# Kernel optimization log

Hardware: AMD Instinct MI355X
Metric: run time of the kernel (lower is better)

The kernel has to match this reference:

```python
import math
import jax, jax.numpy as jnp
import numpy as np

B, S, D = 2, 2048, 1024
N_HEADS, D_KV = 16, 64
INNER = N_HEADS * D_KV
NUM_BUCKETS = 32
MAX_DISTANCE = 128


def _relative_position_bucket(relative_position, num_buckets=NUM_BUCKETS, max_distance=MAX_DISTANCE):
    # bidirectional (encoder) variant
    nb = num_buckets // 2
    rel_buckets = (relative_position > 0).astype(jnp.int32) * nb
    rp = jnp.abs(relative_position)
    max_exact = nb // 2
    is_small = rp < max_exact
    rp_safe = jnp.maximum(rp, 1)  # avoid log(0); selected away by where
    rp_if_large = max_exact + (
        jnp.log(rp_safe.astype(jnp.float32) / max_exact)
        / math.log(max_distance / max_exact)
        * (nb - max_exact)
    ).astype(jnp.int32)
    rp_if_large = jnp.minimum(rp_if_large, nb - 1)
    return rel_buckets + jnp.where(is_small, rp, rp_if_large)


def compute_bias(rel_bias, q_len, k_len):
    ctx = jnp.arange(q_len)[:, None]
    mem = jnp.arange(k_len)[None, :]
    buckets = _relative_position_bucket(mem - ctx)  # [q_len, k_len]
    values = rel_bias[buckets]                      # [q_len, k_len, H]
    return jnp.transpose(values, (2, 0, 1))[None]   # [1, H, q_len, k_len]


def setup_inputs() -> dict:
    key = jax.random.key(0)
    ks = jax.random.split(key, 6)
    s = 1.0 / math.sqrt(D)
    return {
        "hidden_states": jax.random.normal(ks[0], (B, S, D), jnp.float32),
        "wq": jax.random.normal(ks[1], (D, INNER), jnp.float32) * s,
        "wk": jax.random.normal(ks[2], (D, INNER), jnp.float32) * s,
        "wv": jax.random.normal(ks[3], (D, INNER), jnp.float32) * s,
        "wo": jax.random.normal(ks[4], (INNER, D), jnp.float32) * s,
        "rel_bias": jax.random.normal(ks[5], (NUM_BUCKETS, N_HEADS), jnp.float32) * 0.1,
    }


def reference(hidden_states, wq, wk, wv, wo, rel_bias):
    b, s, _ = hidden_states.shape

    def shape(x):  # [b, s, inner] -> [b, h, s, d_kv]
        return x.reshape(b, s, N_HEADS, D_KV).transpose(0, 2, 1, 3)

    q = shape(hidden_states @ wq)  # note: T5 has NO 1/sqrt(d) scaling
    k = shape(hidden_states @ wk)
    v = shape(hidden_states @ wv)

    scores = jnp.einsum("bhqd,bhkd->bhqk", q, k)
    position_bias = compute_bias(rel_bias, s, s)
    scores = scores + position_bias
    attn = jax.nn.softmax(scores.astype(jnp.float32), axis=-1).astype(scores.dtype)

    out = jnp.einsum("bhqk,bhkd->bhqd", attn, v)
    out = out.transpose(0, 2, 1, 3).reshape(b, s, INNER)
    return out @ wo
```

## Files before the change

kernel.cpp:

```cpp
#include <hip/hip_runtime.h>
#include <hip/hip_bf16.h>

#define B_ 2
#define S_ 2048
#define D_ 1024
#define H_ 16
#define DKV_ 64
#define INNER_ 1024
#define M_ (B_*S_)

typedef unsigned short ushort_t;
typedef unsigned int u32;
typedef __bf16 bf16x8 __attribute__((ext_vector_type(8)));
typedef __bf16 bf16x4 __attribute__((ext_vector_type(4)));
typedef float f32x4 __attribute__((ext_vector_type(4)));

#define VMCNT0 asm volatile("s_waitcnt vmcnt(0)" ::: "memory")
#define LOG2E 1.4426950408889634f

__device__ __forceinline__ unsigned short f2bf(float f) {
    unsigned int u = __builtin_bit_cast(unsigned int, f);
    unsigned int r = (u + 0x7fffu + ((u >> 16) & 1u)) >> 16;
    return (unsigned short)r;
}

__device__ __forceinline__ void gload16(const ushort_t* g, ushort_t* l) {
    __builtin_amdgcn_global_load_lds(
        (const __attribute__((address_space(1))) u32*)g,
        (__attribute__((address_space(3))) u32*)l, 16, 0, 0);
}

__global__ __launch_bounds__(256) void cvt_bf16(const float* __restrict__ in,
                                                unsigned short* __restrict__ out, int n) {
    int i = (blockIdx.x * 256 + threadIdx.x) * 4;
    if (i < n) {
        float4 v = *(const float4*)&in[i];
        ushort4 o;
        o.x = f2bf(v.x); o.y = f2bf(v.y); o.z = f2bf(v.z); o.w = f2bf(v.w);
        *(ushort4*)&out[i] = o;
    }
}

__global__ __launch_bounds__(256) void transp_bf16(
        const float* __restrict__ s0, const float* __restrict__ s1,
        const float* __restrict__ s2, const float* __restrict__ s3,
        unsigned short* __restrict__ d0, unsigned short* __restrict__ d1,
        unsigned short* __restrict__ d2, unsigned short* __restrict__ d3) {
    const float* srcs[4] = {s0, s1, s2, s3};
    unsigned short* dsts[4] = {d0, d1, d2, d3};
    const float* src = srcs[blockIdx.z];
    unsigned short* dst = dsts[blockIdx.z];
    __shared__ float t[64][65];
    int k0 = blockIdx.y * 64, n0 = blockIdx.x * 64;
    for (int i = threadIdx.x; i < 4096; i += 256) {
        int r = i >> 6, c = i & 63;
        t[r][c] = src[(k0 + r) * 1024 + n0 + c];
    }
    __syncthreads();
    for (int i = threadIdx.x; i < 4096; i += 256) {
        int r = i >> 6, c = i & 63;
        dst[(n0 + r) * 1024 + k0 + c] = f2bf(t[c][r]);
    }
}

__global__ __launch_bounds__(256) void bias_kernel(const float* __restrict__ rb,
                                                   float* __restrict__ btab) {
    int idx = blockIdx.x * 256 + threadIdx.x;
    int h = idx >> 12, pos = idx & 4095;
    int rel = pos - 2048;
    int bb = rel > 0 ? 16 : 0;
    int rp = rel < 0 ? -rel : rel;
    int bucket;
    if (rp < 8) bucket = bb + rp;
    else {
        int v = 8 + (int)(logf((float)rp * 0.125f) / 2.7725887f * 8.0f);
        bucket = bb + (v < 15 ? v : 15);
    }
    btab[idx] = rb[bucket * 16 + h] * LOG2E;
}

__global__ __launch_bounds__(256) void gemm_qkv(const ushort_t* __restrict__ A,
        const ushort_t* __restrict__ WQ, const ushort_t* __restrict__ WK, const ushort_t* __restrict__ WV,
        ushort_t* __restrict__ Qb, ushort_t* __restrict__ Kb, ushort_t* __restrict__ Vtb) {
    __shared__ alignas(16) ushort_t As[128][64];
    __shared__ alignas(16) ushort_t Bs[128][64];
    int tid = threadIdx.x, wid = tid >> 6, lane = tid & 63;
    int linear = blockIdx.x;
    int swz = (linear & 7) * 96 + (linear >> 3);
    int m0 = (swz / 24) * 128;
    int nblk = swz % 24;
    int sel = nblk >> 3;
    const ushort_t* Bt = sel == 0 ? WQ : (sel == 1 ? WK : WV);
    int n0 = (nblk & 7) * 128;
    int lr = lane & 15, lg = lane >> 4;
    int wm = (wid >> 1) * 64, wn = (wid & 1) * 64;
    int srow = tid >> 3, sp = tid & 7;
    int scol = (sp ^ (srow & 7)) * 8;
    int cR0 = (lg ^ (lr & 7)) * 8;
    int cR1 = ((4 + lg) ^ (lr & 7)) * 8;
    const ushort_t* Abase = A + (size_t)m0 * 1024 + scol;
    const ushort_t* Bbase = Bt + (size_t)n0 * 1024 + scol;
    f32x4 acc[4][4] = {};
    for (int kt = 0; kt < 1024; kt += 64) {
        #pragma unroll
        for (int j = 0; j < 4; ++j) {
            int row = j * 32 + srow;
            gload16(Abase + row * 1024 + kt, &As[0][0] + (j * 256 + tid) * 8);
            gload16(Bbase + row * 1024 + kt, &Bs[0][0] + (j * 256 + tid) * 8);
        }
        VMCNT0;
        __syncthreads();
        bf16x8 af[4][2], bfr[4][2];
        #pragma unroll
        for (int t = 0; t < 4; ++t) {
            af[t][0]  = *(const bf16x8*)&As[wm + t * 16 + lr][cR0];
            af[t][1]  = *(const bf16x8*)&As[wm + t * 16 + lr][cR1];
            bfr[t][0] = *(const bf16x8*)&Bs[wn + t * 16 + lr][cR0];
            bfr[t][1] = *(const bf16x8*)&Bs[wn + t * 16 + lr][cR1];
        }
        #pragma unroll
        for (int hh = 0; hh < 2; ++hh)
            #pragma unroll
            for (int i2 = 0; i2 < 4; ++i2)
                #pragma unroll
                for (int j2 = 0; j2 < 4; ++j2)
                    acc[i2][j2] = __builtin_amdgcn_mfma_f32_16x16x32_bf16(af[i2][hh], bfr[j2][hh], acc[i2][j2], 0, 0, 0);
        __syncthreads();
    }
    #pragma unroll
    for (int i2 = 0; i2 < 4; ++i2)
        #pragma unroll
        for (int j2 = 0; j2 < 4; ++j2) {
            int col = n0 + wn + j2 * 16 + lr;
            int hh = col >> 6, d = col & 63;
            if (sel < 2) {
                ushort_t* dst = sel == 0 ? Qb : Kb;
                #pragma unroll
                for (int r = 0; r < 4; ++r) {
                    int row = m0 + wm + i2 * 16 + lg * 4 + r;
                    int b = row >> 11, s = row & 2047;
                    dst[(((size_t)(b * H_ + hh) * S_ + s)) * DKV_ + d] = f2bf(acc[i2][j2][r]);
                }
            } else {
                int row0 = m0 + wm + i2 * 16 + lg * 4;
                int b = row0 >> 11, s0 = row0 & 2047;
                ushort4 sv;
                sv.x = f2bf(acc[i2][j2][0]); sv.y = f2bf(acc[i2][j2][1]);
                sv.z = f2bf(acc[i2][j2][2]); sv.w = f2bf(acc[i2][j2][3]);
                *(ushort4*)&Vtb[((size_t)(b * H_ + hh) * DKV_ + d) * S_ + s0] = sv;
            }
        }
}

__global__ __launch_bounds__(256) void gemm_out(const ushort_t* __restrict__ A,
                                                const ushort_t* __restrict__ Bt,
                                                float* __restrict__ C) {
    __shared__ alignas(16) ushort_t As[64][64];
    __shared__ alignas(16) ushort_t Bs[128][64];
    int tid = threadIdx.x, wid = tid >> 6, lane = tid & 63;
    int linear = blockIdx.x;
    int swz = (linear & 7) * 64 + (linear >> 3);
    int m0 = (swz >> 3) * 64, n0 = (swz & 7) * 128;
    int lr = lane & 15, lg = lane >> 4;
    int wn = wid * 32;
    int srow = tid >> 3, sp = tid & 7;
    int scol = (sp ^ (srow & 7)) * 8;
    int cR0 = (lg ^ (lr & 7)) * 8;
    int cR1 = ((4 + lg) ^ (lr & 7)) * 8;
    const ushort_t* Abase = A + (size_t)m0 * 1024 + scol;
    const ushort_t* Bbase = Bt + (size_t)n0 * 1024 + scol;
    f32x4 acc[4][2] = {};
    for (int kt = 0; kt < 1024; kt += 64) {
        #pragma unroll
        for (int j = 0; j < 2; ++j) {
            int row = j * 32 + srow;
            gload16(Abase + row * 1024 + kt, &As[0][0] + (j * 256 + tid) * 8);
        }
        #pragma unroll
        for (int j = 0; j < 4; ++j) {
            int row = j * 32 + srow;
            gload16(Bbase + row * 1024 + kt, &Bs[0][0] + (j * 256 + tid) * 8);
        }
        VMCNT0;
        __syncthreads();
        bf16x8 af[4][2], bfr[2][2];
        #pragma unroll
        for (int t = 0; t < 4; ++t) {
            af[t][0] = *(const bf16x8*)&As[t * 16 + lr][cR0];
            af[t][1] = *(const bf16x8*)&As[t * 16 + lr][cR1];
        }
        #pragma unroll
        for (int j = 0; j < 2; ++j) {
            bfr[j][0] = *(const bf16x8*)&Bs[wn + j * 16 + lr][cR0];
            bfr[j][1] = *(const bf16x8*)&Bs[wn + j * 16 + lr][cR1];
        }
        #pragma unroll
        for (int hh = 0; hh < 2; ++hh)
            #pragma unroll
            for (int i2 = 0; i2 < 4; ++i2)
                #pragma unroll
                for (int j2 = 0; j2 < 2; ++j2)
                    acc[i2][j2] = __builtin_amdgcn_mfma_f32_16x16x32_bf16(af[i2][hh], bfr[j2][hh], acc[i2][j2], 0, 0, 0);
        __syncthreads();
    }
    #pragma unroll
    for (int i2 = 0; i2 < 4; ++i2)
        #pragma unroll
        for (int j2 = 0; j2 < 2; ++j2)
            #pragma unroll
            for (int r = 0; r < 4; ++r)
                C[(size_t)(m0 + i2 * 16 + lg * 4 + r) * 1024 + n0 + wn + j2 * 16 + lr] = acc[i2][j2][r];
}

__global__ __launch_bounds__(256) void flash_attn(const ushort_t* __restrict__ Q,
                                                  const ushort_t* __restrict__ Kg,
                                                  const ushort_t* __restrict__ Vt,
                                                  const float* __restrict__ bias_tab,
                                                  ushort_t* __restrict__ Out) {
    __shared__ alignas(16) ushort_t Ks[2][64][64];
    __shared__ alignas(16) ushort_t Vs[2][64][64];
    __shared__ alignas(16) ushort_t Ps[4][16][64];
    __shared__ float LbS[2112];
    int tid = threadIdx.x, wid = tid >> 6, lane = tid & 63;
    int linear = blockIdx.x;
    int swz = (linear & 7) * 128 + (linear >> 3);
    int bh = swz >> 5, qblk = swz & 31;
    int h = bh & 15, b = bh >> 4;
    int q0b = qblk * 64, q0w = q0b + wid * 16;
    int lr = lane & 15, lg = lane >> 4;

    {
        const float* bsrc = bias_tab + h * 4096 + 2048 - q0b - 63;
        for (int i = tid; i < 2111; i += 256) LbS[i] = bsrc[i];
    }

    const ushort_t* Qbase = Q + ((size_t)bh * S_ + q0w) * DKV_;
    bf16x8 qf0 = *(const bf16x8*)&Qbase[lr * DKV_ + lg * 8];
    bf16x8 qf1 = *(const bf16x8*)&Qbase[lr * DKV_ + 32 + lg * 8];

    int srow = tid >> 3, sp = tid & 7;
    int kc = (sp ^ (srow & 7)) * 8;
    const ushort_t* Ksrc = Kg + (size_t)bh * S_ * DKV_ + kc;
    const ushort_t* Vsrc = Vt + (size_t)bh * DKV_ * S_ + kc;
    int c0 = (lg ^ (lr & 7)) * 8;
    int c1 = ((4 + lg) ^ (lr & 7)) * 8;
    int pxor = (lr & 7) << 4;

    f32x4 o[4] = {};
    float mrun = -INFINITY, lrun = 0.f;
    const int bbase = 63 - wid * 16 + 4 * lg - lr;

    auto stage = [&](int bufi, int kt) {
        ushort_t* kb = &Ks[bufi][0][0];
        ushort_t* vb = &Vs[bufi][0][0];
        gload16(Ksrc + (size_t)(kt + srow) * 64,      kb + tid * 8);
        gload16(Ksrc + (size_t)(kt + 32 + srow) * 64, kb + 2048 + tid * 8);
        gload16(Vsrc + (size_t)srow * S_ + kt,        vb + tid * 8);
        gload16(Vsrc + (size_t)(32 + srow) * S_ + kt, vb + 2048 + tid * 8);
    };

    stage(0, 0);
    VMCNT0;
    __syncthreads();
    int buf = 0;
    for (int kt = 0; kt < S_; kt += 64) {
        if (kt + 64 < S_) stage(buf ^ 1, kt + 64);
        f32x4 sa[4] = {};
        #pragma unroll
        for (int nt = 0; nt < 4; ++nt) {
            bf16x8 kf0 = *(const bf16x8*)&Ks[buf][nt * 16 + lr][c0];
            bf16x8 kf1 = *(const bf16x8*)&Ks[buf][nt * 16 + lr][c1];
            sa[nt] = __builtin_amdgcn_mfma_f32_16x16x32_bf16(kf0, qf0, sa[nt], 0, 0, 0);
            sa[nt] = __builtin_amdgcn_mfma_f32_16x16x32_bf16(kf1, qf1, sa[nt], 0, 0, 0);
        }
        float p[4][4];
        float mt = -INFINITY;
        const int bi = kt + bbase;
        #pragma unroll
        for (int nt = 0; nt < 4; ++nt)
            #pragma unroll
            for (int r = 0; r < 4; ++r) {
                float s2 = fmaf(sa[nt][r], LOG2E, LbS[bi + nt * 16 + r]);
                p[nt][r] = s2;
                mt = fmaxf(mt, s2);
            }
        mt = fmaxf(mt, __shfl_xor(mt, 16));
        mt = fmaxf(mt, __shfl_xor(mt, 32));
        if (!__all(mt <= mrun + 8.f)) {
            float mnew = fmaxf(mrun, mt);
            float sc = __builtin_amdgcn_exp2f(mrun - mnew);
            mrun = mnew;
            lrun *= sc;
            #pragma unroll
            for (int dt = 0; dt < 4; ++dt)
                #pragma unroll
                for (int r = 0; r < 4; ++r)
                    o[dt][r] *= sc;
        }
        float psum = 0.f;
        #pragma unroll
        for (int nt = 0; nt < 4; ++nt)
            #pragma unroll
            for (int r = 0; r < 4; ++r) {
                float e = __builtin_amdgcn_exp2f(p[nt][r] - mrun);
                p[nt][r] = e;
                psum += e;
            }
        psum += __shfl_xor(psum, 16);
        psum += __shfl_xor(psum, 32);
        lrun += psum;
        char* pbase = (char*)&Ps[wid][lr][0];
        #pragma unroll
        for (int nt = 0; nt < 4; ++nt) {
            bf16x4 pv;
            pv[0] = (__bf16)p[nt][0]; pv[1] = (__bf16)p[nt][1];
            pv[2] = (__bf16)p[nt][2]; pv[3] = (__bf16)p[nt][3];
            *(bf16x4*)(pbase + ((nt * 32 + lg * 8) ^ pxor)) = pv;
        }
        bf16x8 pf0 = *(const bf16x8*)(pbase + ((lg * 16) ^ pxor));
        bf16x8 pf1 = *(const bf16x8*)(pbase + ((64 + lg * 16) ^ pxor));
        #pragma unroll
        for (int dt = 0; dt < 4; ++dt) {
            bf16x8 vf0 = *(const bf16x8*)&Vs[buf][dt * 16 + lr][c0];
            bf16x8 vf1 = *(const bf16x8*)&Vs[buf][dt * 16 + lr][c1];
            o[dt] = __builtin_amdgcn_mfma_f32_16x16x32_bf16(vf0, pf0, o[dt], 0, 0, 0);
            o[dt] = __builtin_amdgcn_mfma_f32_16x16x32_bf16(vf1, pf1, o[dt], 0, 0, 0);
        }
        VMCNT0;
        __syncthreads();
        buf ^= 1;
    }
    float linv = 1.f / lrun;
    char* pbase = (char*)&Ps[wid][lr][0];
    #pragma unroll
    for (int dt = 0; dt < 4; ++dt) {
        bf16x4 ov;
        ov[0] = (__bf16)(o[dt][0] * linv); ov[1] = (__bf16)(o[dt][1] * linv);
        ov[2] = (__bf16)(o[dt][2] * linv); ov[3] = (__bf16)(o[dt][3] * linv);
        *(bf16x4*)(pbase + ((dt * 32 + lg * 8) ^ pxor)) = ov;
    }
    int row = lane >> 2, seg = lane & 3;
    int rxor = (row & 7) << 4;
    char* rbase = (char*)&Ps[wid][row][0];
    uint4 v0 = *(uint4*)(rbase + ((seg * 32) ^ rxor));
    uint4 v1 = *(uint4*)(rbase + ((seg * 32 + 16) ^ rxor));
    ushort_t* dst = Out + (size_t)(b * S_ + q0w + row) * INNER_ + h * DKV_ + seg * 16;
    *(uint4*)&dst[0] = v0;
    *(uint4*)&dst[8] = v1;
}

extern "C" void kernel_launch(void* const* d_in, const int* in_sizes, int n_in,
                              void* d_out, int out_size, void* d_ws, size_t ws_size,
                              hipStream_t stream) {
    const float* hs = (const float*)d_in[0];
    const float* wq = (const float*)d_in[1];
    const float* wk = (const float*)d_in[2];
    const float* wv = (const float*)d_in[3];
    const float* wo = (const float*)d_in[4];
    const float* rb = (const float*)d_in[5];

    char* ws = (char*)d_ws;
    unsigned short* Abf = (unsigned short*)(ws);
    unsigned short* Wqt = (unsigned short*)(ws + (8u  << 20));
    unsigned short* Wkt = (unsigned short*)(ws + (10u << 20));
    unsigned short* Wvt = (unsigned short*)(ws + (12u << 20));
    unsigned short* Wot = (unsigned short*)(ws + (14u << 20));
    unsigned short* Qb  = (unsigned short*)(ws + (16u << 20));
    unsigned short* Kb  = (unsigned short*)(ws + (24u << 20));
    unsigned short* Vtb = (unsigned short*)(ws + (32u << 20));
    unsigned short* AOb = (unsigned short*)(ws + (40u << 20));
    float*          Btab = (float*)(ws + (48u << 20));

    cvt_bf16<<<4096, 256, 0, stream>>>(hs, Abf, M_ * D_);
    transp_bf16<<<dim3(16, 16, 4), 256, 0, stream>>>(wq, wk, wv, wo, Wqt, Wkt, Wvt, Wot);
    bias_kernel<<<256, 256, 0, stream>>>(rb, Btab);

    gemm_qkv<<<768, 256, 0, stream>>>(Abf, Wqt, Wkt, Wvt, Qb, Kb, Vtb);

    flash_attn<<<1024, 256, 0, stream>>>(Qb, Kb, Vtb, Btab, AOb);

    gemm_out<<<512, 256, 0, stream>>>(AOb, Wot, (float*)d_out);
}
```

Measured before the change: 155.2 us.

## Load V fragments directly from global into registers, bypassing LDS staging

V tiles are no longer staged through shared memory; each wave loads its V^T fragments straight from global memory into registers at the start of each key tile, and only K stays double-buffered in LDS. The row max and exp-sum reductions are also restructured into tree form, with the exp and sum fused into the P store loop. This cuts LDS footprint and LDS traffic and may allow higher occupancy, but each of the four waves now fetches the same V data from global/L2 redundantly. Those loads are issued in the same iteration they are consumed, so their latency is only hidden by the QK^T and softmax work.

```diff
diff --git a/kernel.cpp b/kernel.cpp
--- a/kernel.cpp
+++ b/kernel.cpp
@@ -218,7 +218,6 @@
                                                   const float* __restrict__ bias_tab,
                                                   ushort_t* __restrict__ Out) {
     __shared__ alignas(16) ushort_t Ks[2][64][64];
-    __shared__ alignas(16) ushort_t Vs[2][64][64];
     __shared__ alignas(16) ushort_t Ps[4][16][64];
     __shared__ float LbS[2112];
     int tid = threadIdx.x, wid = tid >> 6, lane = tid & 63;
@@ -241,7 +240,7 @@
     int srow = tid >> 3, sp = tid & 7;
     int kc = (sp ^ (srow & 7)) * 8;
     const ushort_t* Ksrc = Kg + (size_t)bh * S_ * DKV_ + kc;
-    const ushort_t* Vsrc = Vt + (size_t)bh * DKV_ * S_ + kc;
+    const ushort_t* Vfrag = Vt + ((size_t)bh * DKV_ + lr) * S_ + lg * 8;
     int c0 = (lg ^ (lr & 7)) * 8;
     int c1 = ((4 + lg) ^ (lr & 7)) * 8;
     int pxor = (lr & 7) << 4;
@@ -250,21 +249,25 @@
     float mrun = -INFINITY, lrun = 0.f;
     const int bbase = 63 - wid * 16 + 4 * lg - lr;
 
-    auto stage = [&](int bufi, int kt) {
+    auto stageK = [&](int bufi, int kt) {
         ushort_t* kb = &Ks[bufi][0][0];
-        ushort_t* vb = &Vs[bufi][0][0];
         gload16(Ksrc + (size_t)(kt + srow) * 64,      kb + tid * 8);
         gload16(Ksrc + (size_t)(kt + 32 + srow) * 64, kb + 2048 + tid * 8);
-        gload16(Vsrc + (size_t)srow * S_ + kt,        vb + tid * 8);
-        gload16(Vsrc + (size_t)(32 + srow) * S_ + kt, vb + 2048 + tid * 8);
     };
 
-    stage(0, 0);
+    stageK(0, 0);
     VMCNT0;
     __syncthreads();
     int buf = 0;
     for (int kt = 0; kt < S_; kt += 64) {
-        if (kt + 64 < S_) stage(buf ^ 1, kt + 64);
+        bf16x8 vfr[4][2];
+        #pragma unroll
+        for (int dt = 0; dt < 4; ++dt) {
+            const ushort_t* vp = Vfrag + (size_t)dt * 16 * S_ + kt;
+            vfr[dt][0] = *(const bf16x8*)vp;
+            vfr[dt][1] = *(const bf16x8*)(vp + 32);
+        }
+        if (kt + 64 < S_) stageK(buf ^ 1, kt + 64);
         f32x4 sa[4] = {};
         #pragma unroll
         for (int nt = 0; nt < 4; ++nt) {
@@ -274,16 +277,16 @@
             sa[nt] = __builtin_amdgcn_mfma_f32_16x16x32_bf16(kf1, qf1, sa[nt], 0, 0, 0);
         }
         float p[4][4];
-        float mt = -INFINITY;
+        float mnt[4];
         const int bi = kt + bbase;
         #pragma unroll
-        for (int nt = 0; nt < 4; ++nt)
-            #pragma unroll
-            for (int r = 0; r < 4; ++r) {
-                float s2 = fmaf(sa[nt][r], LOG2E, LbS[bi + nt * 16 + r]);
-                p[nt][r] = s2;
-                mt = fmaxf(mt, s2);
-            }
+        for (int nt = 0; nt < 4; ++nt) {
+            #pragma unroll
+            for (int r = 0; r < 4; ++r)
+                p[nt][r] = fmaf(sa[nt][r], LOG2E, LbS[bi + nt * 16 + r]);
+            mnt[nt] = fmaxf(fmaxf(p[nt][0], p[nt][1]), fmaxf(p[nt][2], p[nt][3]));
+        }
+        float mt = fmaxf(fmaxf(mnt[0], mnt[1]), fmaxf(mnt[2], mnt[3]));
         mt = fmaxf(mt, __shfl_xor(mt, 16));
         mt = fmaxf(mt, __shfl_xor(mt, 32));
         if (!__all(mt <= mrun + 8.f)) {
@@ -297,34 +300,29 @@
                 for (int r = 0; r < 4; ++r)
                     o[dt][r] *= sc;
         }
-        float psum = 0.f;
-        #pragma unroll
-        for (int nt = 0; nt < 4; ++nt)
-            #pragma unroll
-            for (int r = 0; r < 4; ++r) {
-                float e = __builtin_amdgcn_exp2f(p[nt][r] - mrun);
-                p[nt][r] = e;
-                psum += e;
-            }
-        psum += __shfl_xor(psum, 16);
-        psum += __shfl_xor(psum, 32);
-        lrun += psum;
         char* pbase = (char*)&Ps[wid][lr][0];
+        float pnt[4];
         #pragma unroll
         for (int nt = 0; nt < 4; ++nt) {
+            #pragma unroll
+            for (int r = 0; r < 4; ++r)
+                p[nt][r] = __builtin_amdgcn_exp2f(p[nt][r] - mrun);
+            pnt[nt] = (p[nt][0] + p[nt][1]) + (p[nt][2] + p[nt][3]);
             bf16x4 pv;
             pv[0] = (__bf16)p[nt][0]; pv[1] = (__bf16)p[nt][1];
             pv[2] = (__bf16)p[nt][2]; pv[3] = (__bf16)p[nt][3];
             *(bf16x4*)(pbase + ((nt * 32 + lg * 8) ^ pxor)) = pv;
         }
+        float psum = (pnt[0] + pnt[1]) + (pnt[2] + pnt[3]);
+        psum += __shfl_xor(psum, 16);
+        psum += __shfl_xor(psum, 32);
+        lrun += psum;
         bf16x8 pf0 = *(const bf16x8*)(pbase + ((lg * 16) ^ pxor));
         bf16x8 pf1 = *(const bf16x8*)(pbase + ((64 + lg * 16) ^ pxor));
         #pragma unroll
         for (int dt = 0; dt < 4; ++dt) {
-            bf16x8 vf0 = *(const bf16x8*)&Vs[buf][dt * 16 + lr][c0];
-            bf16x8 vf1 = *(const bf16x8*)&Vs[buf][dt * 16 + lr][c1];
-            o[dt] = __builtin_amdgcn_mfma_f32_16x16x32_bf16(vf0, pf0, o[dt], 0, 0, 0);
-            o[dt] = __builtin_amdgcn_mfma_f32_16x16x32_bf16(vf1, pf1, o[dt], 0, 0, 0);
+            o[dt] = __builtin_amdgcn_mfma_f32_16x16x32_bf16(vfr[dt][0], pf0, o[dt], 0, 0, 0);
+            o[dt] = __builtin_amdgcn_mfma_f32_16x16x32_bf16(vfr[dt][1], pf1, o[dt], 0, 0, 0);
         }
         VMCNT0;
         __syncthreads();
```

After: 193.4 us. 1.25x slower.
